# Optimization experiments

Hardware: AMD Instinct MI355X
Metric: run time of the kernel (lower is better)

Reference implementation:

```python
import jax, jax.numpy as jnp
import numpy as np

NUM_HEADS = 16

def setup_inputs() -> dict:
    key = jax.random.key(0)
    k1, k2, k3 = jax.random.split(key, 3)
    B, N, C = 4, 2048, 1024
    x = jax.random.normal(k1, (B, N, C), dtype=jnp.float32)
    # torch Linear weights are [out_features, in_features]
    w_qkv = jax.random.normal(k2, (3 * C, C), dtype=jnp.float32) * (1.0 / np.sqrt(C))
    w_out = jax.random.normal(k3, (C, C), dtype=jnp.float32) * (1.0 / np.sqrt(C))
    b_out = jnp.zeros((C,), dtype=jnp.float32)
    return {"x": x, "w_qkv": w_qkv, "w_out": w_out, "b_out": b_out}

def reference(x, w_qkv, w_out, b_out):
    B, N, C = x.shape
    H = NUM_HEADS
    D = C // H
    scale = 1.0 / np.sqrt(D).astype(np.float32)
    # qkv projection: [B,N,3C] -> [3,B,H,N,D]
    qkv = (x @ w_qkv.T).reshape(B, N, 3, H, D).transpose(2, 0, 3, 1, 4)
    q, k, v = qkv[0], qkv[1], qkv[2]
    # The torch module's block-wise online softmax telescopes to exact softmax.
    scores = jnp.einsum("bhqd,bhkd->bhqk", q, k) * scale
    attn = jax.nn.softmax(scores, axis=-1)
    out = jnp.einsum("bhqk,bhkd->bhqd", attn, v)  # [B,H,N,D]
    out = out.transpose(0, 2, 1, 3).reshape(B, N, C)
    return out @ w_out.T + b_out
```

## Files before the change

### kernel.cpp

```cpp
#include <hip/hip_runtime.h>

typedef __attribute__((ext_vector_type(8))) short vbf8;
typedef __attribute__((ext_vector_type(4))) float vf4;

#define GLOAD16(g, l) __builtin_amdgcn_global_load_lds( \
    (const __attribute__((address_space(1))) void*)(g),  \
    (__attribute__((address_space(3))) void*)(l), 16, 0, 0)

__device__ __forceinline__ unsigned short f2bf(float f) {
  union { float f; unsigned u; } v; v.f = f;
  return (unsigned short)((v.u + 0x7fffu + ((v.u >> 16) & 1u)) >> 16);
}

__device__ __forceinline__ unsigned short cvt_bf16(float f) {
  __bf16 h = (__bf16)f;
  union { __bf16 h; unsigned short u; } v; v.h = h;
  return v.u;
}

__device__ __forceinline__ vf4 mfma16(vbf8 a, vbf8 b, vf4 c) {
  return __builtin_amdgcn_mfma_f32_16x16x32_bf16(a, b, c, 0, 0, 0);
}

__device__ __forceinline__ int swz(int row, int col) {
  return row * 64 + (col ^ ((row & 7) << 3));
}

__global__ __launch_bounds__(256)
void k_cvt_bf16(const float* __restrict__ in, unsigned short* __restrict__ out, int n4) {
  for (int i = blockIdx.x * blockDim.x + threadIdx.x; i < n4; i += gridDim.x * blockDim.x) {
    float4 v = ((const float4*)in)[i];
    ushort4 o;
    o.x = f2bf(v.x); o.y = f2bf(v.y); o.z = f2bf(v.z); o.w = f2bf(v.w);
    ((ushort4*)out)[i] = o;
  }
}

__global__ __launch_bounds__(256, 2)
void k_gemm_qkv(const unsigned short* __restrict__ A,
                const unsigned short* __restrict__ B,
                unsigned short* __restrict__ qb,
                unsigned short* __restrict__ kb,
                unsigned short* __restrict__ vb) {
  __shared__ unsigned short As[128 * 64];
  __shared__ unsigned short Bs[128 * 64];
  const int tid = threadIdx.x;
  const int lane = tid & 63;
  const int wid = tid >> 6;
  const int wm = wid >> 1, wn = wid & 1;
  const int flat = blockIdx.y * 24 + blockIdx.x;
  const int sw = (flat & 7) * 192 + (flat >> 3);
  const int m0 = (sw / 24) * 128;
  const int n0 = (sw % 24) * 128;
  const int l15 = lane & 15, kg = lane >> 4;
  const int srow = wid * 32 + (lane >> 3);
  const int scol = (lane & 7) * 8;

  vf4 acc[4][4] = {};

  for (int kt = 0; kt < 16; ++kt) {
    __syncthreads();
    const unsigned short* gA = A + (size_t)(m0 + srow) * 1024 + kt * 64 + scol;
    const unsigned short* gB = B + (size_t)(n0 + srow) * 1024 + kt * 64 + scol;
    const unsigned ab = (unsigned)(wid * 32 * 64);
#pragma unroll
    for (int i = 0; i < 4; ++i) {
      GLOAD16(gA + (size_t)i * 8 * 1024, &As[ab + i * 8 * 64]);
      GLOAD16(gB + (size_t)i * 8 * 1024, &Bs[ab + i * 8 * 64]);
    }
    __syncthreads();
#pragma unroll
    for (int kk = 0; kk < 2; ++kk) {
      vbf8 af[4], bfr[4];
#pragma unroll
      for (int mi = 0; mi < 4; ++mi)
        af[mi] = *(const vbf8*)&As[(wm * 64 + mi * 16 + l15) * 64 + kk * 32 + kg * 8];
#pragma unroll
      for (int ni = 0; ni < 4; ++ni)
        bfr[ni] = *(const vbf8*)&Bs[(wn * 64 + ni * 16 + l15) * 64 + kk * 32 + kg * 8];
#pragma unroll
      for (int mi = 0; mi < 4; ++mi)
#pragma unroll
        for (int ni = 0; ni < 4; ++ni)
          acc[mi][ni] = mfma16(af[mi], bfr[ni], acc[mi][ni]);
    }
  }

#pragma unroll
  for (int ni = 0; ni < 4; ++ni) {
    const int c = n0 + wn * 64 + ni * 16 + l15;
    const int which = c >> 10;
    const int hd = c & 1023;
    unsigned short* dst = (which == 0) ? qb : ((which == 1) ? kb : vb);
    const float sc = (which == 0) ? 0.18033688011112042f : 1.0f;
#pragma unroll
    for (int mi = 0; mi < 4; ++mi) {
#pragma unroll
      for (int r = 0; r < 4; ++r) {
        const int m = m0 + wm * 64 + mi * 16 + kg * 4 + r;
        const int b = m >> 11, nn = m & 2047;
        const size_t idx = (((size_t)(b * 16 + (hd >> 6)) * 2048 + nn) * 64) + (hd & 63);
        dst[idx] = f2bf(acc[mi][ni][r] * sc);
      }
    }
  }
}

__global__ __launch_bounds__(256)
void k_transpose_v(const unsigned short* __restrict__ vb, unsigned short* __restrict__ vt) {
  __shared__ unsigned short t[64][72];
  const int bh = blockIdx.y, n0 = blockIdx.x * 64;
  const int tid = threadIdx.x;
#pragma unroll
  for (int p = 0; p < 2; ++p) {
    const int r = p * 32 + (tid >> 3);
    vbf8 v = *(const vbf8*)&vb[((size_t)bh * 2048 + n0 + r) * 64 + (tid & 7) * 8];
    *(vbf8*)&t[r][(tid & 7) * 8] = v;
  }
  __syncthreads();
  const int d = tid >> 2, jb = (tid & 3) * 16;
  unsigned short buf[16];
#pragma unroll
  for (int j = 0; j < 16; ++j) buf[j] = t[jb + j][d];
  unsigned short* o = &vt[((size_t)bh * 64 + d) * 2048 + n0 + jb];
  *(vbf8*)&o[0] = *(vbf8*)&buf[0];
  *(vbf8*)&o[8] = *(vbf8*)&buf[8];
}

__global__ __launch_bounds__(256, 4)
void k_attn(const unsigned short* __restrict__ qb,
            const unsigned short* __restrict__ kb,
            const unsigned short* __restrict__ vt,
            unsigned short* __restrict__ ob) {
  __shared__ unsigned short Ks[2][64 * 64];
  __shared__ unsigned short Vs[64 * 64];
  __shared__ unsigned short Ps[4][32][64];
  const int tid = threadIdx.x, lane = tid & 63, w = tid >> 6;
  const int l15 = lane & 15, kg = lane >> 4;
  const int flat = blockIdx.x;
  const int sw = (flat & 7) * 128 + (flat >> 3);
  const int qt = sw & 15, bh = sw >> 4;

  const unsigned short* Q = qb + ((size_t)bh * 2048 + qt * 128 + w * 32) * 64;
  vbf8 qf[2][2];
#pragma unroll
  for (int qj = 0; qj < 2; ++qj)
#pragma unroll
    for (int kk = 0; kk < 2; ++kk)
      qf[qj][kk] = *(const vbf8*)(Q + (qj * 16 + l15) * 64 + kk * 32 + kg * 8);

  vbf8 onesv;
#pragma unroll
  for (int i = 0; i < 8; ++i) onesv[i] = (short)0x3F80;

  vf4 oacc[2][4] = {};
  vf4 lacc[2] = {};
  float mrun[2] = {-3.0e38f, -3.0e38f};

  const int srow = lane >> 3;
  const int scol = (((lane & 7) ^ srow) * 8);
  const int pswz = (l15 & 7) << 3;
  const unsigned short* gKbase = kb + ((size_t)bh * 2048 + w * 16 + srow) * 64 + scol;
  const unsigned short* gVbase = vt + ((size_t)bh * 64 + w * 16 + srow) * 2048 + scol;

#define STAGE_K(t, b) do { \
    const unsigned short* gK_ = gKbase + (size_t)(t) * 4096; \
    GLOAD16(gK_,       &Ks[b][(w * 16) * 64]); \
    GLOAD16(gK_ + 512, &Ks[b][(w * 16 + 8) * 64]); \
  } while (0)
#define STAGE_V(t) do { \
    const unsigned short* gV_ = gVbase + (size_t)(t) * 64; \
    GLOAD16(gV_,                 &Vs[(w * 16) * 64]); \
    GLOAD16(gV_ + (size_t)16384, &Vs[(w * 16 + 8) * 64]); \
  } while (0)

  STAGE_K(0, 0);
  asm volatile("s_waitcnt vmcnt(0)" ::: "memory");
  __builtin_amdgcn_s_barrier();
  __builtin_amdgcn_sched_barrier(0);

  for (int kt = 0; kt < 32; ++kt) {
    const int cur = kt & 1;
    STAGE_V(kt);
    if (kt + 1 < 32) STAGE_K(kt + 1, cur ^ 1);

    vf4 s[2][4] = {};
    __builtin_amdgcn_s_setprio(1);
#pragma unroll
    for (int kk = 0; kk < 2; ++kk)
#pragma unroll
      for (int ni = 0; ni < 4; ++ni) {
        const vbf8 kf = *(const vbf8*)&Ks[cur][swz(ni * 16 + l15, kk * 32 + kg * 8)];
        s[0][ni] = mfma16(kf, qf[0][kk], s[0][ni]);
        s[1][ni] = mfma16(kf, qf[1][kk], s[1][ni]);
      }
    __builtin_amdgcn_s_setprio(0);

#pragma unroll
    for (int qj = 0; qj < 2; ++qj) {
      float a0 = fmaxf(fmaxf(s[qj][0][0], s[qj][0][1]), fmaxf(s[qj][0][2], s[qj][0][3]));
      float a1 = fmaxf(fmaxf(s[qj][1][0], s[qj][1][1]), fmaxf(s[qj][1][2], s[qj][1][3]));
      float a2 = fmaxf(fmaxf(s[qj][2][0], s[qj][2][1]), fmaxf(s[qj][2][2], s[qj][2][3]));
      float a3 = fmaxf(fmaxf(s[qj][3][0], s[qj][3][1]), fmaxf(s[qj][3][2], s[qj][3][3]));
      float rm = fmaxf(fmaxf(a0, a1), fmaxf(a2, a3));
      rm = fmaxf(rm, __shfl_xor(rm, 16));
      rm = fmaxf(rm, __shfl_xor(rm, 32));

      if (__any(rm > mrun[qj] + 8.0f)) {
        const float mn = fmaxf(mrun[qj], rm);
        const float alpha = __builtin_amdgcn_exp2f(mrun[qj] - mn);
        mrun[qj] = mn;
        float av[4];
#pragma unroll
        for (int r = 0; r < 4; ++r) av[r] = __shfl(alpha, kg * 4 + r);
#pragma unroll
        for (int r = 0; r < 4; ++r) {
          lacc[qj][r] *= av[r];
#pragma unroll
          for (int ni = 0; ni < 4; ++ni) oacc[qj][ni][r] *= av[r];
        }
      }

#pragma unroll
      for (int ni = 0; ni < 4; ++ni) {
        ushort4 pk;
        pk.x = cvt_bf16(__builtin_amdgcn_exp2f(s[qj][ni][0] - mrun[qj]));
        pk.y = cvt_bf16(__builtin_amdgcn_exp2f(s[qj][ni][1] - mrun[qj]));
        pk.z = cvt_bf16(__builtin_amdgcn_exp2f(s[qj][ni][2] - mrun[qj]));
        pk.w = cvt_bf16(__builtin_amdgcn_exp2f(s[qj][ni][3] - mrun[qj]));
        *(ushort4*)&Ps[w][qj * 16 + l15][(ni * 16 + kg * 4) ^ pswz] = pk;
      }
    }

    if (kt + 1 < 32) asm volatile("s_waitcnt vmcnt(2) lgkmcnt(0)" ::: "memory");
    else             asm volatile("s_waitcnt vmcnt(0) lgkmcnt(0)" ::: "memory");
    __builtin_amdgcn_s_barrier();
    __builtin_amdgcn_sched_barrier(0);

    __builtin_amdgcn_s_setprio(1);
#pragma unroll
    for (int kk = 0; kk < 2; ++kk) {
      const vbf8 pf0 = *(const vbf8*)&Ps[w][l15][(kk * 32 + kg * 8) ^ pswz];
      const vbf8 pf1 = *(const vbf8*)&Ps[w][16 + l15][(kk * 32 + kg * 8) ^ pswz];
      lacc[0] = mfma16(pf0, onesv, lacc[0]);
      lacc[1] = mfma16(pf1, onesv, lacc[1]);
#pragma unroll
      for (int ni = 0; ni < 4; ++ni) {
        const vbf8 vf = *(const vbf8*)&Vs[swz(ni * 16 + l15, kk * 32 + kg * 8)];
        oacc[0][ni] = mfma16(pf0, vf, oacc[0][ni]);
        oacc[1][ni] = mfma16(pf1, vf, oacc[1][ni]);
      }
    }
    __builtin_amdgcn_s_setprio(0);

    __syncthreads();
  }
#undef STAGE_K
#undef STAGE_V

  const int b = bh >> 4, h = bh & 15;
#pragma unroll
  for (int qj = 0; qj < 2; ++qj)
#pragma unroll
    for (int r = 0; r < 4; ++r) {
      const float inv = 1.0f / lacc[qj][r];
      const int q = qt * 128 + w * 32 + qj * 16 + kg * 4 + r;
#pragma unroll
      for (int ni = 0; ni < 4; ++ni)
        ob[((size_t)b * 2048 + q) * 1024 + h * 64 + ni * 16 + l15] = cvt_bf16(oacc[qj][ni][r] * inv);
    }
}

__global__ __launch_bounds__(256, 2)
void k_gemm_out(const unsigned short* __restrict__ A,
                const unsigned short* __restrict__ B,
                const float* __restrict__ bias,
                float* __restrict__ out) {
  __shared__ unsigned short As[128 * 64];
  __shared__ unsigned short Bs[128 * 64];
  const int tid = threadIdx.x;
  const int lane = tid & 63;
  const int wid = tid >> 6;
  const int wm = wid >> 1, wn = wid & 1;
  const int flat = blockIdx.y * 8 + blockIdx.x;
  const int sw = (flat & 7) * 64 + (flat >> 3);
  const int m0 = (sw / 8) * 128;
  const int n0 = (sw % 8) * 128;
  const int l15 = lane & 15, kg = lane >> 4;
  const int srow = wid * 32 + (lane >> 3);
  const int scol = (lane & 7) * 8;

  vf4 acc[4][4] = {};

  for (int kt = 0; kt < 16; ++kt) {
    __syncthreads();
    const unsigned short* gA = A + (size_t)(m0 + srow) * 1024 + kt * 64 + scol;
    const unsigned short* gB = B + (size_t)(n0 + srow) * 1024 + kt * 64 + scol;
    const unsigned ab = (unsigned)(wid * 32 * 64);
#pragma unroll
    for (int i = 0; i < 4; ++i) {
      GLOAD16(gA + (size_t)i * 8 * 1024, &As[ab + i * 8 * 64]);
      GLOAD16(gB + (size_t)i * 8 * 1024, &Bs[ab + i * 8 * 64]);
    }
    __syncthreads();
#pragma unroll
    for (int kk = 0; kk < 2; ++kk) {
      vbf8 af[4], bfr[4];
#pragma unroll
      for (int mi = 0; mi < 4; ++mi)
        af[mi] = *(const vbf8*)&As[(wm * 64 + mi * 16 + l15) * 64 + kk * 32 + kg * 8];
#pragma unroll
      for (int ni = 0; ni < 4; ++ni)
        bfr[ni] = *(const vbf8*)&Bs[(wn * 64 + ni * 16 + l15) * 64 + kk * 32 + kg * 8];
#pragma unroll
      for (int mi = 0; mi < 4; ++mi)
#pragma unroll
        for (int ni = 0; ni < 4; ++ni)
          acc[mi][ni] = mfma16(af[mi], bfr[ni], acc[mi][ni]);
    }
  }

#pragma unroll
  for (int ni = 0; ni < 4; ++ni) {
    const int c = n0 + wn * 64 + ni * 16 + l15;
    const float bv = bias[c];
#pragma unroll
    for (int mi = 0; mi < 4; ++mi) {
#pragma unroll
      for (int r = 0; r < 4; ++r) {
        const int m = m0 + wm * 64 + mi * 16 + kg * 4 + r;
        out[(size_t)m * 1024 + c] = acc[mi][ni][r] + bv;
      }
    }
  }
}

extern "C" void kernel_launch(void* const* d_in, const int* in_sizes, int n_in,
                              void* d_out, int out_size, void* d_ws, size_t ws_size,
                              hipStream_t stream) {
  const float* x     = (const float*)d_in[0];
  const float* w_qkv = (const float*)d_in[1];
  const float* w_out = (const float*)d_in[2];
  const float* b_out = (const float*)d_in[3];
  float* out = (float*)d_out;

  char* ws = (char*)d_ws;
  unsigned short* xbf   = (unsigned short*)(ws);
  unsigned short* wqkvb = (unsigned short*)(ws + 16777216);
  unsigned short* woutb = (unsigned short*)(ws + 23068672);
  unsigned short* qbuf  = (unsigned short*)(ws + 25165824);
  unsigned short* kbuf  = (unsigned short*)(ws + 41943040);
  unsigned short* vbuf  = (unsigned short*)(ws + 58720256);
  unsigned short* vtbuf = (unsigned short*)(ws + 75497472);
  unsigned short* aob   = xbf;

  k_cvt_bf16<<<2048, 256, 0, stream>>>(x, xbf, 8388608 / 4);
  k_cvt_bf16<<<768, 256, 0, stream>>>(w_qkv, wqkvb, 3145728 / 4);
  k_cvt_bf16<<<256, 256, 0, stream>>>(w_out, woutb, 1048576 / 4);

  k_gemm_qkv<<<dim3(24, 64), 256, 0, stream>>>(xbf, wqkvb, qbuf, kbuf, vbuf);
  k_transpose_v<<<dim3(32, 64), 256, 0, stream>>>(vbuf, vtbuf);
  k_attn<<<dim3(1024), 256, 0, stream>>>(qbuf, kbuf, vtbuf, aob);
  k_gemm_out<<<dim3(8, 64), 256, 0, stream>>>(aob, woutb, b_out, out);
}
```

Baseline: 215.4 us.

## Double attention query tile per block to reuse K/V tiles across more rows

Each attention block now handles 256 query rows (64 per wave) instead of 128, so every K and V tile staged in LDS serves twice as many queries and total K/V traffic is halved. The grid shrinks to 512 blocks, and launch bounds drop to 2 blocks per SM to make room for the larger accumulators. K fragments are loaded into registers once and reused across the four query sub-tiles, and the row max uses 3-input max ops. The cost is higher register pressure, a larger P buffer in LDS, fewer resident waves, and only 512 blocks to spread over the GPU, which may leave some compute units underused.

```diff
diff --git a/kernel.cpp b/kernel.cpp
--- a/kernel.cpp
+++ b/kernel.cpp
@@ -20,6 +20,10 @@
 
 __device__ __forceinline__ vf4 mfma16(vbf8 a, vbf8 b, vf4 c) {
   return __builtin_amdgcn_mfma_f32_16x16x32_bf16(a, b, c, 0, 0, 0);
+}
+
+__device__ __forceinline__ float fmax3(float a, float b, float c) {
+  return fmaxf(fmaxf(a, b), c);
 }
 
 __device__ __forceinline__ int swz(int row, int col) {
@@ -127,24 +131,24 @@
   *(vbf8*)&o[8] = *(vbf8*)&buf[8];
 }
 
-__global__ __launch_bounds__(256, 4)
+__global__ __launch_bounds__(256, 2)
 void k_attn(const unsigned short* __restrict__ qb,
             const unsigned short* __restrict__ kb,
             const unsigned short* __restrict__ vt,
             unsigned short* __restrict__ ob) {
   __shared__ unsigned short Ks[2][64 * 64];
   __shared__ unsigned short Vs[64 * 64];
-  __shared__ unsigned short Ps[4][32][64];
+  __shared__ unsigned short Ps[4][64][64];
   const int tid = threadIdx.x, lane = tid & 63, w = tid >> 6;
   const int l15 = lane & 15, kg = lane >> 4;
   const int flat = blockIdx.x;
-  const int sw = (flat & 7) * 128 + (flat >> 3);
-  const int qt = sw & 15, bh = sw >> 4;
-
-  const unsigned short* Q = qb + ((size_t)bh * 2048 + qt * 128 + w * 32) * 64;
-  vbf8 qf[2][2];
-#pragma unroll
-  for (int qj = 0; qj < 2; ++qj)
+  const int sw = (flat & 7) * 64 + (flat >> 3);
+  const int qt = sw & 7, bh = sw >> 3;
+
+  const unsigned short* Q = qb + ((size_t)bh * 2048 + qt * 256 + w * 64) * 64;
+  vbf8 qf[4][2];
+#pragma unroll
+  for (int qj = 0; qj < 4; ++qj)
 #pragma unroll
     for (int kk = 0; kk < 2; ++kk)
       qf[qj][kk] = *(const vbf8*)(Q + (qj * 16 + l15) * 64 + kk * 32 + kg * 8);
@@ -153,9 +157,9 @@
 #pragma unroll
   for (int i = 0; i < 8; ++i) onesv[i] = (short)0x3F80;
 
-  vf4 oacc[2][4] = {};
-  vf4 lacc[2] = {};
-  float mrun[2] = {-3.0e38f, -3.0e38f};
+  vf4 oacc[4][4] = {};
+  vf4 lacc[4] = {};
+  float mrun[4] = {-3.0e38f, -3.0e38f, -3.0e38f, -3.0e38f};
 
   const int srow = lane >> 3;
   const int scol = (((lane & 7) ^ srow) * 8);
@@ -184,25 +188,32 @@
     STAGE_V(kt);
     if (kt + 1 < 32) STAGE_K(kt + 1, cur ^ 1);
 
-    vf4 s[2][4] = {};
-    __builtin_amdgcn_s_setprio(1);
+    vbf8 kfr[2][4];
 #pragma unroll
     for (int kk = 0; kk < 2; ++kk)
 #pragma unroll
-      for (int ni = 0; ni < 4; ++ni) {
-        const vbf8 kf = *(const vbf8*)&Ks[cur][swz(ni * 16 + l15, kk * 32 + kg * 8)];
-        s[0][ni] = mfma16(kf, qf[0][kk], s[0][ni]);
-        s[1][ni] = mfma16(kf, qf[1][kk], s[1][ni]);
-      }
-    __builtin_amdgcn_s_setprio(0);
-
-#pragma unroll
-    for (int qj = 0; qj < 2; ++qj) {
-      float a0 = fmaxf(fmaxf(s[qj][0][0], s[qj][0][1]), fmaxf(s[qj][0][2], s[qj][0][3]));
-      float a1 = fmaxf(fmaxf(s[qj][1][0], s[qj][1][1]), fmaxf(s[qj][1][2], s[qj][1][3]));
-      float a2 = fmaxf(fmaxf(s[qj][2][0], s[qj][2][1]), fmaxf(s[qj][2][2], s[qj][2][3]));
-      float a3 = fmaxf(fmaxf(s[qj][3][0], s[qj][3][1]), fmaxf(s[qj][3][2], s[qj][3][3]));
-      float rm = fmaxf(fmaxf(a0, a1), fmaxf(a2, a3));
+      for (int ni = 0; ni < 4; ++ni)
+        kfr[kk][ni] = *(const vbf8*)&Ks[cur][swz(ni * 16 + l15, kk * 32 + kg * 8)];
+
+#pragma unroll
+    for (int qj = 0; qj < 4; ++qj) {
+      vf4 sq[4] = {};
+      __builtin_amdgcn_s_setprio(1);
+#pragma unroll
+      for (int kk = 0; kk < 2; ++kk)
+#pragma unroll
+        for (int ni = 0; ni < 4; ++ni)
+          sq[ni] = mfma16(kfr[kk][ni], qf[qj][kk], sq[ni]);
+      __builtin_amdgcn_s_setprio(0);
+
+      float rm = fmax3(sq[0][0], sq[0][1], sq[0][2]);
+      rm = fmax3(rm, sq[0][3], sq[1][0]);
+      rm = fmax3(rm, sq[1][1], sq[1][2]);
+      rm = fmax3(rm, sq[1][3], sq[2][0]);
+      rm = fmax3(rm, sq[2][1], sq[2][2]);
+      rm = fmax3(rm, sq[2][3], sq[3][0]);
+      rm = fmax3(rm, sq[3][1], sq[3][2]);
+      rm = fmaxf(rm, sq[3][3]);
       rm = fmaxf(rm, __shfl_xor(rm, 16));
       rm = fmaxf(rm, __shfl_xor(rm, 32));
 
@@ -224,10 +235,10 @@
 #pragma unroll
       for (int ni = 0; ni < 4; ++ni) {
         ushort4 pk;
-        pk.x = cvt_bf16(__builtin_amdgcn_exp2f(s[qj][ni][0] - mrun[qj]));
-        pk.y = cvt_bf16(__builtin_amdgcn_exp2f(s[qj][ni][1] - mrun[qj]));
-        pk.z = cvt_bf16(__builtin_amdgcn_exp2f(s[qj][ni][2] - mrun[qj]));
-        pk.w = cvt_bf16(__builtin_amdgcn_exp2f(s[qj][ni][3] - mrun[qj]));
+        pk.x = cvt_bf16(__builtin_amdgcn_exp2f(sq[ni][0] - mrun[qj]));
+        pk.y = cvt_bf16(__builtin_amdgcn_exp2f(sq[ni][1] - mrun[qj]));
+        pk.z = cvt_bf16(__builtin_amdgcn_exp2f(sq[ni][2] - mrun[qj]));
+        pk.w = cvt_bf16(__builtin_amdgcn_exp2f(sq[ni][3] - mrun[qj]));
         *(ushort4*)&Ps[w][qj * 16 + l15][(ni * 16 + kg * 4) ^ pswz] = pk;
       }
     }
@@ -240,15 +251,19 @@
     __builtin_amdgcn_s_setprio(1);
 #pragma unroll
     for (int kk = 0; kk < 2; ++kk) {
-      const vbf8 pf0 = *(const vbf8*)&Ps[w][l15][(kk * 32 + kg * 8) ^ pswz];
-      const vbf8 pf1 = *(const vbf8*)&Ps[w][16 + l15][(kk * 32 + kg * 8) ^ pswz];
-      lacc[0] = mfma16(pf0, onesv, lacc[0]);
-      lacc[1] = mfma16(pf1, onesv, lacc[1]);
+      vbf8 pf[4];
+#pragma unroll
+      for (int qj = 0; qj < 4; ++qj)
+        pf[qj] = *(const vbf8*)&Ps[w][qj * 16 + l15][(kk * 32 + kg * 8) ^ pswz];
+#pragma unroll
+      for (int qj = 0; qj < 4; ++qj)
+        lacc[qj] = mfma16(pf[qj], onesv, lacc[qj]);
 #pragma unroll
       for (int ni = 0; ni < 4; ++ni) {
         const vbf8 vf = *(const vbf8*)&Vs[swz(ni * 16 + l15, kk * 32 + kg * 8)];
-        oacc[0][ni] = mfma16(pf0, vf, oacc[0][ni]);
-        oacc[1][ni] = mfma16(pf1, vf, oacc[1][ni]);
+#pragma unroll
+        for (int qj = 0; qj < 4; ++qj)
+          oacc[qj][ni] = mfma16(pf[qj], vf, oacc[qj][ni]);
       }
     }
     __builtin_amdgcn_s_setprio(0);
@@ -260,11 +275,11 @@
 
   const int b = bh >> 4, h = bh & 15;
 #pragma unroll
-  for (int qj = 0; qj < 2; ++qj)
+  for (int qj = 0; qj < 4; ++qj)
 #pragma unroll
     for (int r = 0; r < 4; ++r) {
       const float inv = 1.0f / lacc[qj][r];
-      const int q = qt * 128 + w * 32 + qj * 16 + kg * 4 + r;
+      const int q = qt * 256 + w * 64 + qj * 16 + kg * 4 + r;
 #pragma unroll
       for (int ni = 0; ni < 4; ++ni)
         ob[((size_t)b * 2048 + q) * 1024 + h * 64 + ni * 16 + l15] = cvt_bf16(oacc[qj][ni][r] * inv);
@@ -360,6 +375,6 @@
 
   k_gemm_qkv<<<dim3(24, 64), 256, 0, stream>>>(xbf, wqkvb, qbuf, kbuf, vbuf);
   k_transpose_v<<<dim3(32, 64), 256, 0, stream>>>(vbuf, vtbuf);
-  k_attn<<<dim3(1024), 256, 0, stream>>>(qbuf, kbuf, vtbuf, aob);
+  k_attn<<<dim3(512), 256, 0, stream>>>(qbuf, kbuf, vtbuf, aob);
   k_gemm_out<<<dim3(8, 64), 256, 0, stream>>>(aob, woutb, b_out, out);
 }
```

Result: no change. 211.3 us (-1.9%).
